# Performance work log

Measured on AMD Instinct MI355X. Metric: run time of the kernel, lower is better.

Reference implementation:

```python
import jax, jax.numpy as jnp
import numpy as np
import math

B, S, D, H, DH = 1, 2048, 2048, 16, 64  # batch, seq, d_model, n_heads, d_head
LAMBDA_INIT = 0.8
EPS = 1e-5


def setup_inputs() -> dict:
    key = jax.random.key(0)
    ks = jax.random.split(key, 10)
    w_scale = 0.02
    inner = 2 * DH * H  # == D here
    return {
        "x": jax.random.normal(ks[0], (B, S, D), dtype=jnp.float32),
        "Wq": jax.random.normal(ks[1], (D, inner), dtype=jnp.float32) * w_scale,
        "Wk": jax.random.normal(ks[2], (D, inner), dtype=jnp.float32) * w_scale,
        "Wv": jax.random.normal(ks[3], (D, inner), dtype=jnp.float32) * w_scale,
        "Wo": jax.random.normal(ks[4], (inner, D), dtype=jnp.float32) * w_scale,
        "lambda_q1": jax.random.normal(ks[5], (DH,), dtype=jnp.float32) * 0.1,
        "lambda_k1": jax.random.normal(ks[6], (DH,), dtype=jnp.float32) * 0.1,
        "lambda_q2": jax.random.normal(ks[7], (DH,), dtype=jnp.float32) * 0.1,
        "lambda_k2": jax.random.normal(ks[8], (DH,), dtype=jnp.float32) * 0.1,
        "gn_weight": jnp.ones((inner,), dtype=jnp.float32),
        "gn_bias": jnp.zeros((inner,), dtype=jnp.float32),
    }


def reference(x, Wq, Wk, Wv, Wo, lambda_q1, lambda_k1, lambda_q2, lambda_k2,
              gn_weight, gn_bias):
    b, s, _ = x.shape
    dh = lambda_q1.shape[0]
    h = Wq.shape[1] // (2 * dh)
    scale = 1.0 / math.sqrt(dh)

    q = (x @ Wq).reshape(b, s, h, 2, dh)
    k = (x @ Wk).reshape(b, s, h, 2, dh)
    v = (x @ Wv).reshape(b, s, h, 2 * dh)

    # [B,H,S,dh]
    q1 = jnp.swapaxes(q[..., 0, :], 1, 2)
    q2 = jnp.swapaxes(q[..., 1, :], 1, 2)
    k1 = jnp.swapaxes(k[..., 0, :], 1, 2)
    k2 = jnp.swapaxes(k[..., 1, :], 1, 2)
    vh = jnp.swapaxes(v, 1, 2)  # [B,H,S,2*dh]

    score1 = jnp.einsum("bhsd,bhtd->bhst", q1, k1) * scale
    score2 = jnp.einsum("bhsd,bhtd->bhst", q2, k2) * scale
    attn1 = jax.nn.softmax(score1, axis=-1)
    attn2 = jax.nn.softmax(score2, axis=-1)

    lam = (jnp.exp(jnp.sum(lambda_q1 * lambda_k1))
           - jnp.exp(jnp.sum(lambda_q2 * lambda_k2)) + LAMBDA_INIT)

    out = jnp.einsum("bhst,bhtd->bhsd", attn1 - lam * attn2, vh)  # [B,H,S,2dh]
    out = jnp.swapaxes(out, 1, 2)  # [B,S,H,2dh]

    # GroupNorm: n_heads groups over the channel dim, per token
    mu = jnp.mean(out, axis=-1, keepdims=True)
    var = jnp.var(out, axis=-1, keepdims=True)
    out = (out - mu) * jax.lax.rsqrt(var + EPS)
    gw = gn_weight.reshape(h, 2 * dh)
    gb = gn_bias.reshape(h, 2 * dh)
    out = out * gw + gb

    out = out * (1.0 - LAMBDA_INIT)
    return out.reshape(b, s, -1) @ Wo
```

## Files before the change

kernel.cpp:

```cpp
#include <hip/hip_runtime.h>
#include <hip/hip_bf16.h>

typedef unsigned short u16;
typedef __attribute__((ext_vector_type(8))) short short8;
typedef __attribute__((ext_vector_type(4))) short short4v;
typedef __attribute__((ext_vector_type(4))) float f32x4;

#define S_DIM 2048
#define D_DIM 2048
#define H_NUM 16
#define DH_NUM 64

#if __has_builtin(__builtin_amdgcn_exp2f)
#define EXP2(x) __builtin_amdgcn_exp2f(x)
#else
#define EXP2(x) exp2f(x)
#endif

__device__ __forceinline__ u16 f2bf(float f) {
    union { float f; unsigned u; } x; x.f = f;
    unsigned r = x.u + 0x7fff + ((x.u >> 16) & 1);
    return (u16)(r >> 16);
}

__device__ __forceinline__ unsigned pk_bf16(float a, float b) {
    union { __hip_bfloat162 h; unsigned u; } cv;
    float2 t; t.x = a; t.y = b;
    cv.h = __float22bfloat162_rn(t);
    return cv.u;
}

__device__ __forceinline__ void gload16(const void* g, void* l) {
    __builtin_amdgcn_global_load_lds(
        (const __attribute__((address_space(1))) unsigned int*)g,
        (__attribute__((address_space(3))) unsigned int*)l, 16, 0, 0);
}

__device__ __forceinline__ void transpose_body(const float* __restrict__ src,
                                               u16* __restrict__ dst,
                                               int tx, int ty, int t)
{
    __shared__ float tile[64][65];
    const int r0 = ty * 64, c0 = tx * 64;
#pragma unroll
    for (int p = 0; p < 4; ++p) {
        int r = p * 16 + (t >> 4), c = (t & 15) * 4;
        float4 v = *(const float4*)&src[(long)(r0 + r) * D_DIM + c0 + c];
        tile[r][c] = v.x; tile[r][c + 1] = v.y;
        tile[r][c + 2] = v.z; tile[r][c + 3] = v.w;
    }
    __syncthreads();
#pragma unroll
    for (int p = 0; p < 2; ++p) {
        int ch = t + p * 256;
        int i = ch >> 3, j0 = (ch & 7) * 8;
        short8 o;
#pragma unroll
        for (int jj = 0; jj < 8; ++jj)
            o[jj] = (short)f2bf(tile[j0 + jj][i]);
        *(short8*)&dst[(long)(c0 + i) * D_DIM + r0 + j0] = o;
    }
}

__global__ __launch_bounds__(256)
void transpose_fast(const float* __restrict__ src, u16* __restrict__ dst)
{
    transpose_body(src, dst, blockIdx.x, blockIdx.y, threadIdx.x);
}

__global__ __launch_bounds__(256)
void prep4(const float* __restrict__ x,
           const float* __restrict__ Wq, const float* __restrict__ Wk,
           const float* __restrict__ Wv,
           u16* __restrict__ XB, u16* T0, u16* T1, u16* T2)
{
    const int z = blockIdx.z, t = threadIdx.x, bx = blockIdx.x;
    if (z == 0) {
        long i0 = ((long)bx * 256 + t) * 16;
        short8 o0, o1;
#pragma unroll
        for (int j = 0; j < 2; ++j) {
            float4 a = *(const float4*)&x[i0 + j * 8];
            float4 b = *(const float4*)&x[i0 + j * 8 + 4];
            short8& o = j ? o1 : o0;
            o[0] = (short)f2bf(a.x); o[1] = (short)f2bf(a.y);
            o[2] = (short)f2bf(a.z); o[3] = (short)f2bf(a.w);
            o[4] = (short)f2bf(b.x); o[5] = (short)f2bf(b.y);
            o[6] = (short)f2bf(b.z); o[7] = (short)f2bf(b.w);
        }
        *(short8*)&XB[i0] = o0;
        *(short8*)&XB[i0 + 8] = o1;
    } else {
        const float* src = (z == 1) ? Wq : (z == 2) ? Wk : Wv;
        u16* dst         = (z == 1) ? T0 : (z == 2) ? T1 : T2;
        transpose_body(src, dst, bx & 31, bx >> 5, t);
    }
}

__global__ __launch_bounds__(256)
void cvt_bf16(const float* __restrict__ src, u16* __restrict__ dst)
{
    int i = (blockIdx.x * 256 + threadIdx.x) * 4;
    float4 v = *(const float4*)(src + i);
    ushort4 o;
    o.x = f2bf(v.x); o.y = f2bf(v.y); o.z = f2bf(v.z); o.w = f2bf(v.w);
    *(ushort4*)(dst + i) = o;
}

__global__ __launch_bounds__(256, 2)
void gemm128(const u16* __restrict__ A,
             const u16* B0, const u16* B1, const u16* B2,
             u16* C0, u16* C1, u16* C2, int zbase)
{
    const int Kd = D_DIM, N = D_DIM, M = S_DIM;
    const int z = blockIdx.z + zbase;
    const u16* Bt = (z == 0) ? B0 : (z == 1) ? B1 : B2;
    u16* C        = (z == 0) ? C0 : (z == 1) ? C1 : C2;

    __shared__ __attribute__((aligned(16))) u16 As[128 * 32];
    __shared__ __attribute__((aligned(16))) u16 Bs[128 * 32];

    const int tid = threadIdx.x, lane = tid & 63, wave = tid >> 6;
    const int bm = blockIdx.x * 128, bn = blockIdx.y * 128;

    const int lrow = lane >> 2;
    const int gchunk = (lane & 3) ^ ((lane >> 3) & 3);
    const long aoff0 = (long)(bm + wave * 32 + lrow) * Kd + gchunk * 8;
    const long aoff1 = aoff0 + 16L * Kd;
    const long boff0 = (long)(bn + wave * 32 + lrow) * Kd + gchunk * 8;
    const long boff1 = boff0 + 16L * Kd;
    u16* as0 = &As[wave * 1024];
    u16* as1 = &As[wave * 1024 + 512];
    u16* bs0 = &Bs[wave * 1024];
    u16* bs1 = &Bs[wave * 1024 + 512];

    const int wr = (wave >> 1) * 64, wc = (wave & 1) * 64;
    const int fr = lane & 15, fq = lane >> 4;

    f32x4 acc[4][4];
    for (int i = 0; i < 4; ++i)
        for (int j = 0; j < 4; ++j) { f32x4 zz = {0.f,0.f,0.f,0.f}; acc[i][j] = zz; }

    for (int k0 = 0; k0 < Kd; k0 += 32) {
        gload16(A + aoff0 + k0, as0);
        gload16(A + aoff1 + k0, as1);
        gload16(Bt + boff0 + k0, bs0);
        gload16(Bt + boff1 + k0, bs1);
        __syncthreads();

        short8 af[4], bf[4];
#pragma unroll
        for (int i = 0; i < 4; ++i) {
            int m = wr + i * 16 + fr;
            int slot = fq ^ ((m >> 1) & 3);
            af[i] = *(const short8*)&As[m * 32 + slot * 8];
            int n = wc + i * 16 + fr;
            int slotb = fq ^ ((n >> 1) & 3);
            bf[i] = *(const short8*)&Bs[n * 32 + slotb * 8];
        }
        if (z == 2) {
#pragma unroll
            for (int i = 0; i < 4; ++i)
#pragma unroll
                for (int j = 0; j < 4; ++j)
                    acc[i][j] = __builtin_amdgcn_mfma_f32_16x16x32_bf16(bf[j], af[i], acc[i][j], 0, 0, 0);
        } else {
#pragma unroll
            for (int i = 0; i < 4; ++i)
#pragma unroll
                for (int j = 0; j < 4; ++j)
                    acc[i][j] = __builtin_amdgcn_mfma_f32_16x16x32_bf16(af[i], bf[j], acc[i][j], 0, 0, 0);
        }
        __syncthreads();
    }

    if (z == 2) {
#pragma unroll
        for (int i = 0; i < 4; ++i) {
            int tok = bm + wr + i * 16 + fr;
#pragma unroll
            for (int j = 0; j < 4; ++j) {
                int ch = bn + wc + j * 16 + fq * 4;
#pragma unroll
                for (int r = 0; r < 4; ++r)
                    C[(long)(ch + r) * M + tok] = f2bf(acc[i][j][r]);
            }
        }
    } else {
        const float sc = (z == 0) ? 0.125f * 1.44269504f : 1.0f;
#pragma unroll
        for (int i = 0; i < 4; ++i) {
            int row = bm + wr + i * 16 + fq * 4;
#pragma unroll
            for (int j = 0; j < 4; ++j) {
                int col = bn + wc + j * 16 + fr;
#pragma unroll
                for (int r = 0; r < 4; ++r)
                    C[(long)(row + r) * N + col] = f2bf(acc[i][j][r] * sc);
            }
        }
    }
}

__global__ __launch_bounds__(256, 2)
void gemm_out(const u16* __restrict__ A, const u16* __restrict__ Bt,
              float* __restrict__ C)
{
    const int Kd = D_DIM, N = D_DIM;

    __shared__ __attribute__((aligned(16))) u16 As[64 * 32];
    __shared__ __attribute__((aligned(16))) u16 Bs[128 * 32];

    const int tid = threadIdx.x, lane = tid & 63, wave = tid >> 6;
    const int bm = blockIdx.x * 64, bn = blockIdx.y * 128;

    const int lrow = lane >> 2;
    const int gchunk = (lane & 3) ^ ((lane >> 3) & 3);
    const long aoff  = (long)(bm + wave * 16 + lrow) * Kd + gchunk * 8;
    const long boff0 = (long)(bn + wave * 32 + lrow) * Kd + gchunk * 8;
    const long boff1 = boff0 + 16L * Kd;
    u16* as  = &As[wave * 512];
    u16* bs0 = &Bs[wave * 1024];
    u16* bs1 = &Bs[wave * 1024 + 512];

    const int wr = (wave >> 1) * 32, wc = (wave & 1) * 64;
    const int fr = lane & 15, fq = lane >> 4;

    f32x4 acc[2][4];
    for (int i = 0; i < 2; ++i)
        for (int j = 0; j < 4; ++j) { f32x4 zz = {0.f,0.f,0.f,0.f}; acc[i][j] = zz; }

    for (int k0 = 0; k0 < Kd; k0 += 32) {
        gload16(A + aoff + k0, as);
        gload16(Bt + boff0 + k0, bs0);
        gload16(Bt + boff1 + k0, bs1);
        __syncthreads();

        short8 af[2], bf[4];
#pragma unroll
        for (int i = 0; i < 2; ++i) {
            int m = wr + i * 16 + fr;
            int slot = fq ^ ((m >> 1) & 3);
            af[i] = *(const short8*)&As[m * 32 + slot * 8];
        }
#pragma unroll
        for (int j = 0; j < 4; ++j) {
            int n = wc + j * 16 + fr;
            int slotb = fq ^ ((n >> 1) & 3);
            bf[j] = *(const short8*)&Bs[n * 32 + slotb * 8];
        }
#pragma unroll
        for (int i = 0; i < 2; ++i)
#pragma unroll
            for (int j = 0; j < 4; ++j)
                acc[i][j] = __builtin_amdgcn_mfma_f32_16x16x32_bf16(af[i], bf[j], acc[i][j], 0, 0, 0);
        __syncthreads();
    }

#pragma unroll
    for (int i = 0; i < 2; ++i) {
        int row = bm + wr + i * 16 + fq * 4;
#pragma unroll
        for (int j = 0; j < 4; ++j) {
            int col = bn + wc + j * 16 + fr;
#pragma unroll
            for (int r = 0; r < 4; ++r)
                C[(long)(row + r) * N + col] = acc[i][j][r];
        }
    }
}

__global__ __launch_bounds__(256, 2)
void diff_attn(const u16* __restrict__ Qm, const u16* __restrict__ Km,
               const u16* __restrict__ Vt,
               const float* __restrict__ lq1, const float* __restrict__ lk1,
               const float* __restrict__ lq2, const float* __restrict__ lk2,
               const float* __restrict__ gw, const float* __restrict__ gb,
               u16* __restrict__ Y)
{
    __shared__ __attribute__((aligned(16))) u16 K1s[2][64 * 72];
    __shared__ __attribute__((aligned(16))) u16 K2s[2][64 * 72];
    __shared__ __attribute__((aligned(16))) u16 Vts[2][128 * 72];

    const int tid = threadIdx.x, lane = tid & 63, wave = tid >> 6;
    const int h = blockIdx.y;
    const int q0 = blockIdx.x * 64 + wave * 16;
    const int fr = lane & 15, qq = lane >> 4;

    float d1 = 0.f, d2 = 0.f;
    for (int i = 0; i < DH_NUM; ++i) {
        d1 += lq1[i] * lk1[i];
        d2 += lq2[i] * lk2[i];
    }
    const float lam = __expf(d1) - __expf(d2) + 0.8f;

    short8 q1f[2], q2f[2];
    {
        const u16* qb = Qm + (long)(q0 + fr) * D_DIM + h * 128;
        q1f[0] = *(const short8*)(qb + qq * 8);
        q1f[1] = *(const short8*)(qb + 32 + qq * 8);
        q2f[0] = *(const short8*)(qb + 64 + qq * 8);
        q2f[1] = *(const short8*)(qb + 96 + qq * 8);
    }

    f32x4 a1[8], a2[8];
    for (int n = 0; n < 8; ++n) { f32x4 zz = {0.f,0.f,0.f,0.f}; a1[n] = zz; a2[n] = zz; }
    float ls1 = 0.f, ls2 = 0.f;

    const int t0 = tid >> 3, c0 = tid & 7;
    short8 k1r[2], k2r[2], vr[4];

    auto load_tile = [&](int kb) {
        const long krow = (long)(kb * 64) * D_DIM + h * 128;
        k1r[0] = *(const short8*)&Km[krow + (long)t0 * D_DIM + c0 * 8];
        k2r[0] = *(const short8*)&Km[krow + (long)t0 * D_DIM + 64 + c0 * 8];
        k1r[1] = *(const short8*)&Km[krow + (long)(t0 + 32) * D_DIM + c0 * 8];
        k2r[1] = *(const short8*)&Km[krow + (long)(t0 + 32) * D_DIM + 64 + c0 * 8];
#pragma unroll
        for (int it = 0; it < 4; ++it)
            vr[it] = *(const short8*)&Vt[(long)(h * 128 + t0 + it * 32) * S_DIM + kb * 64 + c0 * 8];
    };
    auto store_tile = [&](int b) {
        *(short8*)&K1s[b][t0 * 72 + c0 * 8] = k1r[0];
        *(short8*)&K2s[b][t0 * 72 + c0 * 8] = k2r[0];
        *(short8*)&K1s[b][(t0 + 32) * 72 + c0 * 8] = k1r[1];
        *(short8*)&K2s[b][(t0 + 32) * 72 + c0 * 8] = k2r[1];
#pragma unroll
        for (int it = 0; it < 4; ++it)
            *(short8*)&Vts[b][(t0 + it * 32) * 72 + c0 * 8] = vr[it];
    };

    load_tile(0);
    store_tile(0);
    int p = 0;

    for (int kb = 0; kb < S_DIM / 64; ++kb) {
        __syncthreads();
        const bool more = (kb + 1 < S_DIM / 64);
        if (more) load_tile(kb + 1);

#pragma unroll
        for (int j = 0; j < 4; ++j) {
            f32x4 s1 = {0.f,0.f,0.f,0.f}, s2 = {0.f,0.f,0.f,0.f};
#pragma unroll
            for (int ks = 0; ks < 2; ++ks) {
                short8 k1 = *(const short8*)&K1s[p][(j * 16 + fr) * 72 + ks * 32 + qq * 8];
                short8 k2 = *(const short8*)&K2s[p][(j * 16 + fr) * 72 + ks * 32 + qq * 8];
                s1 = __builtin_amdgcn_mfma_f32_16x16x32_bf16(k1, q1f[ks], s1, 0, 0, 0);
                s2 = __builtin_amdgcn_mfma_f32_16x16x32_bf16(k2, q2f[ks], s2, 0, 0, 0);
            }
            float e1[4], e2[4];
#pragma unroll
            for (int r = 0; r < 4; ++r) {
                e1[r] = EXP2(s1[r]);
                e2[r] = EXP2(s2[r]);
                ls1 += e1[r]; ls2 += e2[r];
            }
            union { short4v s; unsigned u[2]; } P1, P2;
            P1.u[0] = pk_bf16(e1[0], e1[1]); P1.u[1] = pk_bf16(e1[2], e1[3]);
            P2.u[0] = pk_bf16(e2[0], e2[1]); P2.u[1] = pk_bf16(e2[2], e2[3]);
#pragma unroll
            for (int n = 0; n < 8; ++n) {
                short4v vf = *(const short4v*)&Vts[p][(n * 16 + fr) * 72 + j * 16 + qq * 4];
                a1[n] = __builtin_amdgcn_mfma_f32_16x16x16bf16_1k(vf, P1.s, a1[n], 0, 0, 0);
                a2[n] = __builtin_amdgcn_mfma_f32_16x16x16bf16_1k(vf, P2.s, a2[n], 0, 0, 0);
            }
        }

        if (more) store_tile(p ^ 1);
        p ^= 1;
    }

    float L1 = ls1, L2 = ls2;
    L1 += __shfl_xor(L1, 16, 64); L1 += __shfl_xor(L1, 32, 64);
    L2 += __shfl_xor(L2, 16, 64); L2 += __shfl_xor(L2, 32, 64);
    const float i1 = 1.f / L1, i2 = lam / L2;

    float o[8][4], sum = 0.f, sq = 0.f;
#pragma unroll
    for (int n = 0; n < 8; ++n)
#pragma unroll
        for (int r = 0; r < 4; ++r) {
            float v = a1[n][r] * i1 - a2[n][r] * i2;
            o[n][r] = v; sum += v; sq += v * v;
        }
    sum += __shfl_xor(sum, 16, 64); sum += __shfl_xor(sum, 32, 64);
    sq  += __shfl_xor(sq, 16, 64);  sq  += __shfl_xor(sq, 32, 64);
    const float mean = sum * (1.f / 128.f);
    const float var = sq * (1.f / 128.f) - mean * mean;
    const float inv = rsqrtf(var + 1e-5f);

    const long yrow = (long)(q0 + fr) * D_DIM + h * 128;
#pragma unroll
    for (int n = 0; n < 8; ++n) {
        float4 g4 = *(const float4*)&gw[h * 128 + n * 16 + qq * 4];
        float4 b4 = *(const float4*)&gb[h * 128 + n * 16 + qq * 4];
        ushort4 st;
        st.x = f2bf(((o[n][0] - mean) * inv * g4.x + b4.x) * 0.2f);
        st.y = f2bf(((o[n][1] - mean) * inv * g4.y + b4.y) * 0.2f);
        st.z = f2bf(((o[n][2] - mean) * inv * g4.z + b4.z) * 0.2f);
        st.w = f2bf(((o[n][3] - mean) * inv * g4.w + b4.w) * 0.2f);
        *(ushort4*)&Y[yrow + n * 16 + qq * 4] = st;
    }
}

extern "C" void kernel_launch(void* const* d_in, const int* in_sizes, int n_in,
                              void* d_out, int out_size, void* d_ws, size_t ws_size,
                              hipStream_t stream)
{
    const float* x   = (const float*)d_in[0];
    const float* Wq  = (const float*)d_in[1];
    const float* Wk  = (const float*)d_in[2];
    const float* Wv  = (const float*)d_in[3];
    const float* Wo  = (const float*)d_in[4];
    const float* lq1 = (const float*)d_in[5];
    const float* lk1 = (const float*)d_in[6];
    const float* lq2 = (const float*)d_in[7];
    const float* lk2 = (const float*)d_in[8];
    const float* gw  = (const float*)d_in[9];
    const float* gb  = (const float*)d_in[10];

    char* ws = (char*)d_ws;
    const size_t SEG = (size_t)D_DIM * D_DIM * sizeof(u16);
    const dim3 tgrid(32, 32), agrid(32, 16), ogrid(32, 16);

    if (ws_size >= 7 * SEG) {
        u16* XB  = (u16*)(ws + 0 * SEG);
        u16* WTq = (u16*)(ws + 1 * SEG);
        u16* WTk = (u16*)(ws + 2 * SEG);
        u16* WTv = (u16*)(ws + 3 * SEG);
        u16* Qb  = (u16*)(ws + 4 * SEG);
        u16* Kb  = (u16*)(ws + 5 * SEG);
        u16* Vt  = (u16*)(ws + 6 * SEG);
        u16* WTo = WTq;
        u16* Yb  = WTk;

        prep4<<<dim3(1024, 1, 4), 256, 0, stream>>>(x, Wq, Wk, Wv,
                                                    XB, WTq, WTk, WTv);
        gemm128<<<dim3(16, 16, 3), 256, 0, stream>>>(XB, WTq, WTk, WTv,
                                                     Qb, Kb, Vt, 0);
        transpose_fast<<<tgrid, 256, 0, stream>>>(Wo, WTo);
        diff_attn<<<agrid, 256, 0, stream>>>(Qb, Kb, Vt, lq1, lk1, lq2, lk2,
                                             gw, gb, Yb);
        gemm_out<<<ogrid, 256, 0, stream>>>(Yb, WTo, (float*)d_out);
    } else {
        u16* XB = (u16*)(ws + 0 * SEG);
        u16* WT = (u16*)(ws + 1 * SEG);
        u16* Qb = (u16*)(ws + 2 * SEG);
        u16* Kb = (u16*)(ws + 3 * SEG);
        u16* Vt = (u16*)(ws + 4 * SEG);

        cvt_bf16<<<4096, 256, 0, stream>>>(x, XB);
        transpose_fast<<<tgrid, 256, 0, stream>>>(Wq, WT);
        gemm128<<<dim3(16, 16, 1), 256, 0, stream>>>(XB, WT, WT, WT, Qb, Qb, Qb, 0);
        transpose_fast<<<tgrid, 256, 0, stream>>>(Wk, WT);
        gemm128<<<dim3(16, 16, 1), 256, 0, stream>>>(XB, WT, WT, WT, Kb, Kb, Kb, 1);
        transpose_fast<<<tgrid, 256, 0, stream>>>(Wv, WT);
        gemm128<<<dim3(16, 16, 1), 256, 0, stream>>>(XB, WT, WT, WT, Vt, Vt, Vt, 2);
        diff_attn<<<agrid, 256, 0, stream>>>(Qb, Kb, Vt, lq1, lk1, lq2, lk2,
                                             gw, gb, XB);
        transpose_fast<<<tgrid, 256, 0, stream>>>(Wo, WT);
        gemm_out<<<ogrid, 256, 0, stream>>>(XB, WT, (float*)d_out);
    }
}
```

Baseline: 330.5 us.

## Double query tile per wave and stream K/V tiles directly into swizzled LDS

The attention kernel now handles 128 queries per block (32 per wave, two 16-row M tiles), so each K and V fragment read from shared memory feeds twice as many MFMAs. Tile loads switch from register staging plus explicit stores to direct global-to-LDS loads (gload16) with an XOR swizzle in place of row padding. This removes the register round trip and halves K/V traffic per query. The cost is roughly double the accumulator registers, so launch bounds drop to one block per CU and the grid halves to 256 blocks, which may lower occupancy and latency hiding.

Result: slower. 348.6 us (+5.5%).

```diff
diff --git a/kernel.cpp b/kernel.cpp
--- a/kernel.cpp
+++ b/kernel.cpp
@@ -270,7 +270,7 @@
     }
 }
 
-__global__ __launch_bounds__(256, 2)
+__global__ __launch_bounds__(256, 1)
 void diff_attn(const u16* __restrict__ Qm, const u16* __restrict__ Km,
                const u16* __restrict__ Vt,
                const float* __restrict__ lq1, const float* __restrict__ lk1,
@@ -278,13 +278,13 @@
                const float* __restrict__ gw, const float* __restrict__ gb,
                u16* __restrict__ Y)
 {
-    __shared__ __attribute__((aligned(16))) u16 K1s[2][64 * 72];
-    __shared__ __attribute__((aligned(16))) u16 K2s[2][64 * 72];
-    __shared__ __attribute__((aligned(16))) u16 Vts[2][128 * 72];
+    __shared__ __attribute__((aligned(16))) u16 K1s[2][64 * 64];
+    __shared__ __attribute__((aligned(16))) u16 K2s[2][64 * 64];
+    __shared__ __attribute__((aligned(16))) u16 Vts[2][128 * 64];
 
     const int tid = threadIdx.x, lane = tid & 63, wave = tid >> 6;
     const int h = blockIdx.y;
-    const int q0 = blockIdx.x * 64 + wave * 16;
+    const int q0 = blockIdx.x * 128 + wave * 32;
     const int fr = lane & 15, qq = lane >> 4;
 
     float d1 = 0.f, d2 = 0.f;
@@ -294,113 +294,139 @@
     }
     const float lam = __expf(d1) - __expf(d2) + 0.8f;
 
-    short8 q1f[2], q2f[2];
-    {
-        const u16* qb = Qm + (long)(q0 + fr) * D_DIM + h * 128;
-        q1f[0] = *(const short8*)(qb + qq * 8);
-        q1f[1] = *(const short8*)(qb + 32 + qq * 8);
-        q2f[0] = *(const short8*)(qb + 64 + qq * 8);
-        q2f[1] = *(const short8*)(qb + 96 + qq * 8);
-    }
-
-    f32x4 a1[8], a2[8];
-    for (int n = 0; n < 8; ++n) { f32x4 zz = {0.f,0.f,0.f,0.f}; a1[n] = zz; a2[n] = zz; }
-    float ls1 = 0.f, ls2 = 0.f;
-
-    const int t0 = tid >> 3, c0 = tid & 7;
-    short8 k1r[2], k2r[2], vr[4];
-
-    auto load_tile = [&](int kb) {
+    short8 q1f[2][2], q2f[2][2];
+#pragma unroll
+    for (int mt = 0; mt < 2; ++mt) {
+        const u16* qb = Qm + (long)(q0 + mt * 16 + fr) * D_DIM + h * 128;
+        q1f[mt][0] = *(const short8*)(qb + qq * 8);
+        q1f[mt][1] = *(const short8*)(qb + 32 + qq * 8);
+        q2f[mt][0] = *(const short8*)(qb + 64 + qq * 8);
+        q2f[mt][1] = *(const short8*)(qb + 96 + qq * 8);
+    }
+
+    f32x4 a1[2][8], a2[2][8];
+    for (int mt = 0; mt < 2; ++mt)
+        for (int n = 0; n < 8; ++n) { f32x4 zz = {0.f,0.f,0.f,0.f}; a1[mt][n] = zz; a2[mt][n] = zz; }
+    float ls1[2] = {0.f, 0.f}, ls2[2] = {0.f, 0.f};
+
+    const int grow = lane >> 3;
+    const int gcol = ((lane & 7) ^ grow) * 8;
+
+    auto fill = [&](int kb, int b) {
         const long krow = (long)(kb * 64) * D_DIM + h * 128;
-        k1r[0] = *(const short8*)&Km[krow + (long)t0 * D_DIM + c0 * 8];
-        k2r[0] = *(const short8*)&Km[krow + (long)t0 * D_DIM + 64 + c0 * 8];
-        k1r[1] = *(const short8*)&Km[krow + (long)(t0 + 32) * D_DIM + c0 * 8];
-        k2r[1] = *(const short8*)&Km[krow + (long)(t0 + 32) * D_DIM + 64 + c0 * 8];
-#pragma unroll
-        for (int it = 0; it < 4; ++it)
-            vr[it] = *(const short8*)&Vt[(long)(h * 128 + t0 + it * 32) * S_DIM + kb * 64 + c0 * 8];
+#pragma unroll
+        for (int g = 0; g < 2; ++g) {
+            int t = wave * 16 + g * 8 + grow;
+            gload16(Km + krow + (long)t * D_DIM + gcol,
+                    &K1s[b][(wave * 16 + g * 8) * 64]);
+            gload16(Km + krow + (long)t * D_DIM + 64 + gcol,
+                    &K2s[b][(wave * 16 + g * 8) * 64]);
+        }
+#pragma unroll
+        for (int g = 0; g < 4; ++g) {
+            int ch = wave * 32 + g * 8 + grow;
+            gload16(Vt + (long)(h * 128 + ch) * S_DIM + kb * 64 + gcol,
+                    &Vts[b][(wave * 32 + g * 8) * 64]);
+        }
     };
-    auto store_tile = [&](int b) {
-        *(short8*)&K1s[b][t0 * 72 + c0 * 8] = k1r[0];
-        *(short8*)&K2s[b][t0 * 72 + c0 * 8] = k2r[0];
-        *(short8*)&K1s[b][(t0 + 32) * 72 + c0 * 8] = k1r[1];
-        *(short8*)&K2s[b][(t0 + 32) * 72 + c0 * 8] = k2r[1];
-#pragma unroll
-        for (int it = 0; it < 4; ++it)
-            *(short8*)&Vts[b][(t0 + it * 32) * 72 + c0 * 8] = vr[it];
-    };
-
-    load_tile(0);
-    store_tile(0);
+
+    const int swz = fr & 7;
+    const int kc0 = ((qq ^ swz) * 8);
+    const int kc1 = (((4 + qq) ^ swz) * 8);
+    int vo[4];
+#pragma unroll
+    for (int j = 0; j < 4; ++j)
+        vo[j] = (((j * 2 + (qq >> 1)) ^ swz) * 8) + (qq & 1) * 4;
+
+    fill(0, 0);
     int p = 0;
 
     for (int kb = 0; kb < S_DIM / 64; ++kb) {
         __syncthreads();
-        const bool more = (kb + 1 < S_DIM / 64);
-        if (more) load_tile(kb + 1);
+        if (kb + 1 < S_DIM / 64) fill(kb + 1, p ^ 1);
 
 #pragma unroll
         for (int j = 0; j < 4; ++j) {
-            f32x4 s1 = {0.f,0.f,0.f,0.f}, s2 = {0.f,0.f,0.f,0.f};
-#pragma unroll
-            for (int ks = 0; ks < 2; ++ks) {
-                short8 k1 = *(const short8*)&K1s[p][(j * 16 + fr) * 72 + ks * 32 + qq * 8];
-                short8 k2 = *(const short8*)&K2s[p][(j * 16 + fr) * 72 + ks * 32 + qq * 8];
-                s1 = __builtin_amdgcn_mfma_f32_16x16x32_bf16(k1, q1f[ks], s1, 0, 0, 0);
-                s2 = __builtin_amdgcn_mfma_f32_16x16x32_bf16(k2, q2f[ks], s2, 0, 0, 0);
-            }
-            float e1[4], e2[4];
+            const int rowK = (j * 16 + fr) * 64;
+            f32x4 s1[2], s2[2];
+            { f32x4 zz = {0.f,0.f,0.f,0.f}; s1[0]=zz; s1[1]=zz; s2[0]=zz; s2[1]=zz; }
+            {
+                short8 k1 = *(const short8*)&K1s[p][rowK + kc0];
+                short8 k2 = *(const short8*)&K2s[p][rowK + kc0];
+#pragma unroll
+                for (int mt = 0; mt < 2; ++mt) {
+                    s1[mt] = __builtin_amdgcn_mfma_f32_16x16x32_bf16(k1, q1f[mt][0], s1[mt], 0, 0, 0);
+                    s2[mt] = __builtin_amdgcn_mfma_f32_16x16x32_bf16(k2, q2f[mt][0], s2[mt], 0, 0, 0);
+                }
+            }
+            {
+                short8 k1 = *(const short8*)&K1s[p][rowK + kc1];
+                short8 k2 = *(const short8*)&K2s[p][rowK + kc1];
+#pragma unroll
+                for (int mt = 0; mt < 2; ++mt) {
+                    s1[mt] = __builtin_amdgcn_mfma_f32_16x16x32_bf16(k1, q1f[mt][1], s1[mt], 0, 0, 0);
+                    s2[mt] = __builtin_amdgcn_mfma_f32_16x16x32_bf16(k2, q2f[mt][1], s2[mt], 0, 0, 0);
+                }
+            }
+            union { short4v s; unsigned u[2]; } P1[2], P2[2];
+#pragma unroll
+            for (int mt = 0; mt < 2; ++mt) {
+                float e1[4], e2[4];
+#pragma unroll
+                for (int r = 0; r < 4; ++r) {
+                    e1[r] = EXP2(s1[mt][r]);
+                    e2[r] = EXP2(s2[mt][r]);
+                    ls1[mt] += e1[r]; ls2[mt] += e2[r];
+                }
+                P1[mt].u[0] = pk_bf16(e1[0], e1[1]); P1[mt].u[1] = pk_bf16(e1[2], e1[3]);
+                P2[mt].u[0] = pk_bf16(e2[0], e2[1]); P2[mt].u[1] = pk_bf16(e2[2], e2[3]);
+            }
+#pragma unroll
+            for (int n = 0; n < 8; ++n) {
+                short4v vf = *(const short4v*)&Vts[p][(n * 16 + fr) * 64 + vo[j]];
+#pragma unroll
+                for (int mt = 0; mt < 2; ++mt) {
+                    a1[mt][n] = __builtin_amdgcn_mfma_f32_16x16x16bf16_1k(vf, P1[mt].s, a1[mt][n], 0, 0, 0);
+                    a2[mt][n] = __builtin_amdgcn_mfma_f32_16x16x16bf16_1k(vf, P2[mt].s, a2[mt][n], 0, 0, 0);
+                }
+            }
+        }
+        p ^= 1;
+    }
+
+#pragma unroll
+    for (int mt = 0; mt < 2; ++mt) {
+        float L1 = ls1[mt], L2 = ls2[mt];
+        L1 += __shfl_xor(L1, 16, 64); L1 += __shfl_xor(L1, 32, 64);
+        L2 += __shfl_xor(L2, 16, 64); L2 += __shfl_xor(L2, 32, 64);
+        const float i1 = 1.f / L1, i2 = lam / L2;
+
+        float o[8][4], sum = 0.f, sq = 0.f;
+#pragma unroll
+        for (int n = 0; n < 8; ++n)
 #pragma unroll
             for (int r = 0; r < 4; ++r) {
-                e1[r] = EXP2(s1[r]);
-                e2[r] = EXP2(s2[r]);
-                ls1 += e1[r]; ls2 += e2[r];
-            }
-            union { short4v s; unsigned u[2]; } P1, P2;
-            P1.u[0] = pk_bf16(e1[0], e1[1]); P1.u[1] = pk_bf16(e1[2], e1[3]);
-            P2.u[0] = pk_bf16(e2[0], e2[1]); P2.u[1] = pk_bf16(e2[2], e2[3]);
-#pragma unroll
-            for (int n = 0; n < 8; ++n) {
-                short4v vf = *(const short4v*)&Vts[p][(n * 16 + fr) * 72 + j * 16 + qq * 4];
-                a1[n] = __builtin_amdgcn_mfma_f32_16x16x16bf16_1k(vf, P1.s, a1[n], 0, 0, 0);
-                a2[n] = __builtin_amdgcn_mfma_f32_16x16x16bf16_1k(vf, P2.s, a2[n], 0, 0, 0);
-            }
-        }
-
-        if (more) store_tile(p ^ 1);
-        p ^= 1;
-    }
-
-    float L1 = ls1, L2 = ls2;
-    L1 += __shfl_xor(L1, 16, 64); L1 += __shfl_xor(L1, 32, 64);
-    L2 += __shfl_xor(L2, 16, 64); L2 += __shfl_xor(L2, 32, 64);
-    const float i1 = 1.f / L1, i2 = lam / L2;
-
-    float o[8][4], sum = 0.f, sq = 0.f;
-#pragma unroll
-    for (int n = 0; n < 8; ++n)
-#pragma unroll
-        for (int r = 0; r < 4; ++r) {
-            float v = a1[n][r] * i1 - a2[n][r] * i2;
-            o[n][r] = v; sum += v; sq += v * v;
-        }
-    sum += __shfl_xor(sum, 16, 64); sum += __shfl_xor(sum, 32, 64);
-    sq  += __shfl_xor(sq, 16, 64);  sq  += __shfl_xor(sq, 32, 64);
-    const float mean = sum * (1.f / 128.f);
-    const float var = sq * (1.f / 128.f) - mean * mean;
-    const float inv = rsqrtf(var + 1e-5f);
-
-    const long yrow = (long)(q0 + fr) * D_DIM + h * 128;
-#pragma unroll
-    for (int n = 0; n < 8; ++n) {
-        float4 g4 = *(const float4*)&gw[h * 128 + n * 16 + qq * 4];
-        float4 b4 = *(const float4*)&gb[h * 128 + n * 16 + qq * 4];
-        ushort4 st;
-        st.x = f2bf(((o[n][0] - mean) * inv * g4.x + b4.x) * 0.2f);
-        st.y = f2bf(((o[n][1] - mean) * inv * g4.y + b4.y) * 0.2f);
-        st.z = f2bf(((o[n][2] - mean) * inv * g4.z + b4.z) * 0.2f);
-        st.w = f2bf(((o[n][3] - mean) * inv * g4.w + b4.w) * 0.2f);
-        *(ushort4*)&Y[yrow + n * 16 + qq * 4] = st;
+                float v = a1[mt][n][r] * i1 - a2[mt][n][r] * i2;
+                o[n][r] = v; sum += v; sq += v * v;
+            }
+        sum += __shfl_xor(sum, 16, 64); sum += __shfl_xor(sum, 32, 64);
+        sq  += __shfl_xor(sq, 16, 64);  sq  += __shfl_xor(sq, 32, 64);
+        const float mean = sum * (1.f / 128.f);
+        const float var = sq * (1.f / 128.f) - mean * mean;
+        const float inv = rsqrtf(var + 1e-5f);
+
+        const long yrow = (long)(q0 + mt * 16 + fr) * D_DIM + h * 128;
+#pragma unroll
+        for (int n = 0; n < 8; ++n) {
+            float4 g4 = *(const float4*)&gw[h * 128 + n * 16 + qq * 4];
+            float4 b4 = *(const float4*)&gb[h * 128 + n * 16 + qq * 4];
+            ushort4 st;
+            st.x = f2bf(((o[n][0] - mean) * inv * g4.x + b4.x) * 0.2f);
+            st.y = f2bf(((o[n][1] - mean) * inv * g4.y + b4.y) * 0.2f);
+            st.z = f2bf(((o[n][2] - mean) * inv * g4.z + b4.z) * 0.2f);
+            st.w = f2bf(((o[n][3] - mean) * inv * g4.w + b4.w) * 0.2f);
+            *(ushort4*)&Y[yrow + n * 16 + qq * 4] = st;
+        }
     }
 }
 
@@ -422,7 +448,7 @@
 
     char* ws = (char*)d_ws;
     const size_t SEG = (size_t)D_DIM * D_DIM * sizeof(u16);
-    const dim3 tgrid(32, 32), agrid(32, 16), ogrid(32, 16);
+    const dim3 tgrid(32, 32), agrid(16, 16), ogrid(32, 16);
 
     if (ws_size >= 7 * SEG) {
         u16* XB  = (u16*)(ws + 0 * SEG);
```
